# Kernel optimization log

Measured on AMD Instinct MI355X. Metric: run time of the kernel, lower is better.

Reference implementation:

```python
import jax, jax.numpy as jnp
import numpy as np
from jax import lax

B, T = 64, 2048
ENC, DEC, ATT = 512, 1024, 128
NFILT, KSIZE = 32, 31
PAD = KSIZE // 2


def setup_inputs() -> dict:
    key = jax.random.key(0)
    ks = jax.random.split(key, 9)
    query = jax.random.normal(ks[0], (B, 1, DEC), dtype=jnp.float32)
    keys = jax.random.normal(ks[1], (B, T, ENC), dtype=jnp.float32)
    prev_weights = jax.random.uniform(ks[2], (B, T), dtype=jnp.float32)
    mask = jax.random.randint(ks[3], (B, T), 0, 2, dtype=jnp.int32)
    # params stored as [in, out] (transpose of torch Linear weight); same math
    W1 = jax.random.normal(ks[4], (ENC, ATT), dtype=jnp.float32) * (ENC ** -0.5)
    W2 = jax.random.normal(ks[5], (DEC, ATT), dtype=jnp.float32) * (DEC ** -0.5)
    V = jax.random.normal(ks[6], (ATT,), dtype=jnp.float32) * (ATT ** -0.5)
    conv_w = jax.random.normal(ks[7], (NFILT, 1, KSIZE), dtype=jnp.float32) * (KSIZE ** -0.5)
    loc_dense = jax.random.normal(ks[8], (NFILT, ATT), dtype=jnp.float32) * (NFILT ** -0.5)
    return {"query": query, "keys": keys, "prev_weights": prev_weights, "mask": mask,
            "W1": W1, "W2": W2, "V": V, "conv_w": conv_w, "loc_dense": loc_dense}


def reference(query, keys, prev_weights, mask, W1, W2, V, conv_w, loc_dense):
    proj_key = jnp.einsum('bte,ea->bta', keys, W1)          # [B,T,A]
    proj_query = jnp.einsum('bqd,da->bqa', query, W2)       # [B,1,A]
    # location conv: input [B,1,T], kernel [F,1,K], 'same' padding -> [B,F,T]
    loc_feat = lax.conv_general_dilated(prev_weights[:, None, :], conv_w,
                                        window_strides=(1,), padding=[(PAD, PAD)],
                                        dimension_numbers=('NCH', 'OIH', 'NCH'))
    proj_loc = jnp.einsum('bft,fa->bta', loc_feat, loc_dense)  # [B,T,A]
    scores = jnp.einsum('bta,a->bt', jnp.tanh(proj_key + proj_query + proj_loc), V)
    scores = jnp.where(mask == 0, -1e9, scores)
    weights = jax.nn.softmax(scores, axis=-1)                # [B,T]
    context = jnp.einsum('bt,bte->be', weights, keys)[:, None, :]  # [B,1,ENC]
    return context, weights
```

## Files before the change

### kernel.cpp

```cpp
#include <hip/hip_runtime.h>

typedef __attribute__((ext_vector_type(4))) float f32x4;
typedef __attribute__((ext_vector_type(8))) short bf16x8;

#define T_LEN 2048
#define ENC   512
#define DEC   1024
#define ATT   128
#define NB    64
#define BM    128
#define BK    32
#define NXB   (T_LEN / BM)
#define NSTEP 17

typedef unsigned int u32;
typedef __attribute__((address_space(1))) const u32 gu32;
typedef __attribute__((address_space(3))) u32 lu32;

__device__ __forceinline__ void async_copy16(const float* g, float* l) {
  __builtin_amdgcn_global_load_lds((gu32*)g, (lu32*)l, 16, 0, 0);
}

__device__ __forceinline__ unsigned short f2bf_rne(float x) {
  unsigned int u = __builtin_bit_cast(unsigned int, x);
  u += 0x7fff + ((u >> 16) & 1);
  return (unsigned short)(u >> 16);
}
__device__ __forceinline__ short f2bf_fast(float x) {
  unsigned int u = __builtin_bit_cast(unsigned int, x);
  return (short)((u + 0x8000u) >> 16);
}

__device__ __forceinline__ float fast_tanh(float x) {
  float e = __expf(2.f * x);
  return 1.f - 2.f / (e + 1.f);
}

__global__ __launch_bounds__(128) void prep(
    const float* __restrict__ query, const float* __restrict__ W2,
    const float* __restrict__ W1, const float* __restrict__ convw,
    const float* __restrict__ ldense,
    float* __restrict__ pq, unsigned short* __restrict__ Bl) {
  int bidx = blockIdx.x;
  if (bidx < NB) {
    int a = threadIdx.x;
    float acc = 0.f;
    for (int d = 0; d < DEC; ++d) acc += query[bidx * DEC + d] * W2[d * ATT + a];
    pq[bidx * ATT + a] = acc;
  } else {
    int a = bidx - NB;
    for (int k = threadIdx.x; k < NSTEP * BK; k += 128) {
      float v = 0.f;
      if (k < 512) {
        v = W1[k * ATT + a];
      } else if (k < 543) {
        int kc = k - 512;
        #pragma unroll
        for (int f = 0; f < 32; ++f) v += convw[f * 31 + kc] * ldense[f * ATT + a];
      }
      int kt = k >> 5, kk = k & 31;
      Bl[(kt * 128 + a) * BK + kk] = f2bf_rne(v);
    }
  }
}

__global__ __launch_bounds__(256, 4) void lsa_main(
    const float* __restrict__ keys, const float* __restrict__ prev,
    const int* __restrict__ mask, const unsigned short* __restrict__ Bl,
    const float* __restrict__ pq, const float* __restrict__ Vv,
    float* __restrict__ wout, float* __restrict__ dpart, float* __restrict__ cpart) {
  __shared__ float Abf[2][BM * BK];
  __shared__ float s_red[2][BM];
  __shared__ float e_vals[BM];

  const int tid = threadIdx.x;
  const int b = blockIdx.y;
  const int trow0 = blockIdx.x * BM;
  const int bid = b * NXB + blockIdx.x;

  const int lane = tid & 63;
  const int w = tid >> 6;
  const int wr = w >> 1, wc = w & 1;
  const int rsel = lane & 15, grp = lane >> 4;

  const int lr = lane >> 3, cp = lane & 7;
  const int gr = w * 32 + lr;
  const int gc = cp ^ lr;
  const float* gA = keys + ((size_t)b * T_LEN + trow0 + gr) * ENC + gc * 4;

  const unsigned short* gB = Bl + (size_t)(wc * 64 + rsel) * BK + grp * 8;

  const int rx = rsel & 7;
  const int ca0 = (2 * grp) ^ rx, ca1 = (2 * grp + 1) ^ rx;
  const int arow_base = (wr * 64 + rsel) * BK;

  f32x4 acc[4][4];
  #pragma unroll
  for (int m = 0; m < 4; ++m)
    #pragma unroll
    for (int n = 0; n < 4; ++n) acc[m][n] = (f32x4)0.f;

  #pragma unroll
  for (int i = 0; i < 4; ++i)
    async_copy16(gA + (size_t)i * 8 * ENC, &Abf[0][(w * 4 + i) * 256]);
  __syncthreads();

  for (int t = 0; t < 16; ++t) {
    if (t < 15) {
      const float* gt = gA + (t + 1) * BK;
      float* dst = &Abf[(t + 1) & 1][0];
      #pragma unroll
      for (int i = 0; i < 4; ++i)
        async_copy16(gt + (size_t)i * 8 * ENC, &dst[(w * 4 + i) * 256]);
    } else {
      const int r = tid >> 1, kh = tid & 1;
      const int rx2 = r & 7;
      float* dst = &Abf[0][r * BK];
      #pragma unroll
      for (int jc = 0; jc < 4; ++jc) {
        int c = kh * 4 + jc;
        f32x4 v;
        #pragma unroll
        for (int q = 0; q < 4; ++q) {
          int kk = c * 4 + q;
          int pos = trow0 + r + kk - 15;
          v[q] = (kk < 31 && pos >= 0 && pos < T_LEN) ? prev[b * T_LEN + pos] : 0.f;
        }
        *reinterpret_cast<f32x4*>(&dst[(c ^ rx2) * 4]) = v;
      }
    }
    bf16x8 bfr[4];
    {
      const unsigned short* gBt = gB + (size_t)t * (128 * BK);
      #pragma unroll
      for (int n = 0; n < 4; ++n)
        bfr[n] = *reinterpret_cast<const bf16x8*>(gBt + n * 16 * BK);
    }
    {
      const float* Ab = &Abf[t & 1][0];
      #pragma unroll
      for (int m = 0; m < 4; ++m) {
        f32x4 x0 = *reinterpret_cast<const f32x4*>(&Ab[arow_base + m * 16 * BK + ca0 * 4]);
        f32x4 x1 = *reinterpret_cast<const f32x4*>(&Ab[arow_base + m * 16 * BK + ca1 * 4]);
        bf16x8 af;
        #pragma unroll
        for (int j = 0; j < 4; ++j) { af[j] = f2bf_fast(x0[j]); af[4 + j] = f2bf_fast(x1[j]); }
        #pragma unroll
        for (int n = 0; n < 4; ++n)
          acc[m][n] = __builtin_amdgcn_mfma_f32_16x16x32_bf16(af, bfr[n], acc[m][n], 0, 0, 0);
      }
    }
    __syncthreads();
  }
  {
    bf16x8 bfr[4];
    const unsigned short* gBt = gB + (size_t)16 * (128 * BK);
    #pragma unroll
    for (int n = 0; n < 4; ++n)
      bfr[n] = *reinterpret_cast<const bf16x8*>(gBt + n * 16 * BK);
    const float* Ab = &Abf[0][0];
    #pragma unroll
    for (int m = 0; m < 4; ++m) {
      f32x4 x0 = *reinterpret_cast<const f32x4*>(&Ab[arow_base + m * 16 * BK + ca0 * 4]);
      f32x4 x1 = *reinterpret_cast<const f32x4*>(&Ab[arow_base + m * 16 * BK + ca1 * 4]);
      bf16x8 af;
      #pragma unroll
      for (int j = 0; j < 4; ++j) { af[j] = f2bf_fast(x0[j]); af[4 + j] = f2bf_fast(x1[j]); }
      #pragma unroll
      for (int n = 0; n < 4; ++n)
        acc[m][n] = __builtin_amdgcn_mfma_f32_16x16x32_bf16(af, bfr[n], acc[m][n], 0, 0, 0);
    }
  }

  float psum[4][4];
  #pragma unroll
  for (int m = 0; m < 4; ++m)
    #pragma unroll
    for (int i = 0; i < 4; ++i) psum[m][i] = 0.f;
  #pragma unroll
  for (int n = 0; n < 4; ++n) {
    int c = wc * 64 + n * 16 + rsel;
    float pqv = pq[b * ATT + c];
    float vv = Vv[c];
    #pragma unroll
    for (int m = 0; m < 4; ++m)
      #pragma unroll
      for (int i = 0; i < 4; ++i)
        psum[m][i] += vv * fast_tanh(acc[m][n][i] + pqv);
  }
  #pragma unroll
  for (int m = 0; m < 4; ++m)
    #pragma unroll
    for (int i = 0; i < 4; ++i) {
      float v = psum[m][i];
      v += __shfl_xor(v, 1, 64);
      v += __shfl_xor(v, 2, 64);
      v += __shfl_xor(v, 4, 64);
      v += __shfl_xor(v, 8, 64);
      psum[m][i] = v;
    }
  if (rsel == 0) {
    #pragma unroll
    for (int m = 0; m < 4; ++m)
      #pragma unroll
      for (int i = 0; i < 4; ++i)
        s_red[wc][wr * 64 + m * 16 + grp * 4 + i] = psum[m][i];
  }
  __syncthreads();

  if (tid < BM) {
    int trow = trow0 + tid;
    float s = s_red[0][tid] + s_red[1][tid];
    float e = (mask[b * T_LEN + trow] == 0) ? 0.f : __expf(s);
    wout[b * T_LEN + trow] = e;
    e_vals[tid] = e;
  }
  __syncthreads();

  if (tid < 64) {
    float v = e_vals[tid] + e_vals[tid + 64];
    #pragma unroll
    for (int off = 32; off; off >>= 1) v += __shfl_xor(v, off, 64);
    if (tid == 0) dpart[bid] = v;
  }

  float c0 = 0.f, c1 = 0.f;
  const float* krow = keys + ((size_t)b * T_LEN + trow0) * ENC;
  #pragma unroll 4
  for (int r = 0; r < BM; ++r) {
    float e = e_vals[r];
    if (e != 0.f) {
      c0 += e * krow[(size_t)r * ENC + tid];
      c1 += e * krow[(size_t)r * ENC + tid + 256];
    }
  }
  cpart[(size_t)bid * ENC + tid] = c0;
  cpart[(size_t)bid * ENC + tid + 256] = c1;
}

__global__ __launch_bounds__(256) void lsa_finalize(
    const float* __restrict__ dpart, const float* __restrict__ cpart,
    float* __restrict__ out) {
  int b = blockIdx.x, tid = threadIdx.x;
  float d = 0.f;
  #pragma unroll
  for (int i = 0; i < NXB; ++i) d += dpart[b * NXB + i];
  float inv = 1.f / d;
  for (int e = tid; e < ENC; e += 256) {
    float c = 0.f;
    #pragma unroll
    for (int i = 0; i < NXB; ++i) c += cpart[((size_t)(b * NXB + i)) * ENC + e];
    out[b * ENC + e] = c * inv;
  }
  float* wrow = out + NB * ENC + (size_t)b * T_LEN;
  for (int t = tid; t < T_LEN; t += 256) wrow[t] *= inv;
}

extern "C" void kernel_launch(void* const* d_in, const int* in_sizes, int n_in,
                              void* d_out, int out_size, void* d_ws, size_t ws_size,
                              hipStream_t stream) {
  const float* query  = (const float*)d_in[0];
  const float* keys   = (const float*)d_in[1];
  const float* prev   = (const float*)d_in[2];
  const int*   mask   = (const int*)d_in[3];
  const float* W1     = (const float*)d_in[4];
  const float* W2     = (const float*)d_in[5];
  const float* V      = (const float*)d_in[6];
  const float* convw  = (const float*)d_in[7];
  const float* ldense = (const float*)d_in[8];
  float* out = (float*)d_out;

  char* ws = (char*)d_ws;
  unsigned short* Bl = (unsigned short*)ws;
  float* pq    = (float*)(ws + 139264);
  float* dpart = (float*)(ws + 139264 + 32768);
  float* cpart = (float*)(ws + 139264 + 32768 + 4096);

  prep<<<dim3(192), dim3(128), 0, stream>>>(query, W2, W1, convw, ldense, pq, Bl);
  dim3 grid(NXB, NB);
  lsa_main<<<grid, dim3(256), 0, stream>>>(keys, prev, mask, Bl, pq, V,
                                           out + NB * ENC, dpart, cpart);
  lsa_finalize<<<dim3(NB), dim3(256), 0, stream>>>(dpart, cpart, out);
}
```

Measured before the change: 135.5 us.

## Unroll GEMM K-loop by two with register-prefetched B fragments; vectorize context accumulation

The main K loop is unrolled by two with ping-pong register buffers for the B fragments, so the next step's B loads are issued before the current MFMA block runs. The context pass now loads two adjacent floats per thread with a vector load and drops the branch that skipped masked rows. The query projection in prep is split across four accumulators to shorten its dependency chain. The changes trade extra registers and code size for better latency hiding, and the context pass now also reads keys for masked rows.

Measured after the change: 134.9 us. Within noise of the previous version (-0.4%).

```diff
diff --git a/kernel.cpp b/kernel.cpp
--- a/kernel.cpp
+++ b/kernel.cpp
@@ -1,6 +1,7 @@
 #include <hip/hip_runtime.h>
 
 typedef __attribute__((ext_vector_type(4))) float f32x4;
+typedef __attribute__((ext_vector_type(2))) float f32x2;
 typedef __attribute__((ext_vector_type(8))) short bf16x8;
 
 #define T_LEN 2048
@@ -11,7 +12,6 @@
 #define BM    128
 #define BK    32
 #define NXB   (T_LEN / BM)
-#define NSTEP 17
 
 typedef unsigned int u32;
 typedef __attribute__((address_space(1))) const u32 gu32;
@@ -44,12 +44,18 @@
   int bidx = blockIdx.x;
   if (bidx < NB) {
     int a = threadIdx.x;
-    float acc = 0.f;
-    for (int d = 0; d < DEC; ++d) acc += query[bidx * DEC + d] * W2[d * ATT + a];
-    pq[bidx * ATT + a] = acc;
+    const float* q = query + bidx * DEC;
+    float a0 = 0.f, a1 = 0.f, a2 = 0.f, a3 = 0.f;
+    for (int d = 0; d < DEC; d += 4) {
+      a0 += q[d]     * W2[(d)     * ATT + a];
+      a1 += q[d + 1] * W2[(d + 1) * ATT + a];
+      a2 += q[d + 2] * W2[(d + 2) * ATT + a];
+      a3 += q[d + 3] * W2[(d + 3) * ATT + a];
+    }
+    pq[bidx * ATT + a] = (a0 + a1) + (a2 + a3);
   } else {
     int a = bidx - NB;
-    for (int k = threadIdx.x; k < NSTEP * BK; k += 128) {
+    for (int k = threadIdx.x; k < 17 * BK; k += 128) {
       float v = 0.f;
       if (k < 512) {
         v = W1[k * ATT + a];
@@ -100,77 +106,68 @@
     #pragma unroll
     for (int n = 0; n < 4; ++n) acc[m][n] = (f32x4)0.f;
 
-  #pragma unroll
-  for (int i = 0; i < 4; ++i)
-    async_copy16(gA + (size_t)i * 8 * ENC, &Abf[0][(w * 4 + i) * 256]);
+#define STAGE(t_, buf_) do { \
+    const float* gt_ = gA + (t_) * BK; \
+    float* dst_ = &Abf[buf_][0]; \
+    _Pragma("unroll") \
+    for (int i_ = 0; i_ < 4; ++i_) \
+      async_copy16(gt_ + (size_t)i_ * 8 * ENC, &dst_[(w * 4 + i_) * 256]); } while (0)
+
+#define STAGE_CONV() do { \
+    const int r_ = tid >> 1, kh_ = tid & 1; \
+    const int rx2_ = r_ & 7; \
+    float* dst_ = &Abf[0][r_ * BK]; \
+    _Pragma("unroll") \
+    for (int jc_ = 0; jc_ < 4; ++jc_) { \
+      int c_ = kh_ * 4 + jc_; \
+      f32x4 v_; \
+      _Pragma("unroll") \
+      for (int q_ = 0; q_ < 4; ++q_) { \
+        int kk_ = c_ * 4 + q_; \
+        int pos_ = trow0 + r_ + kk_ - 15; \
+        v_[q_] = (kk_ < 31 && pos_ >= 0 && pos_ < T_LEN) ? prev[b * T_LEN + pos_] : 0.f; \
+      } \
+      *reinterpret_cast<f32x4*>(&dst_[(c_ ^ rx2_) * 4]) = v_; \
+    } } while (0)
+
+#define LOADB(dst_, t_) do { \
+    const unsigned short* gBt_ = gB + (size_t)(t_) * (128 * BK); \
+    dst_[0] = *reinterpret_cast<const bf16x8*>(gBt_); \
+    dst_[1] = *reinterpret_cast<const bf16x8*>(gBt_ + 16 * BK); \
+    dst_[2] = *reinterpret_cast<const bf16x8*>(gBt_ + 32 * BK); \
+    dst_[3] = *reinterpret_cast<const bf16x8*>(gBt_ + 48 * BK); } while (0)
+
+#define COMPUTE(buf_, br_) do { \
+    const float* Ab_ = &Abf[buf_][0]; \
+    _Pragma("unroll") \
+    for (int m_ = 0; m_ < 4; ++m_) { \
+      f32x4 x0_ = *reinterpret_cast<const f32x4*>(&Ab_[arow_base + m_ * 16 * BK + ca0 * 4]); \
+      f32x4 x1_ = *reinterpret_cast<const f32x4*>(&Ab_[arow_base + m_ * 16 * BK + ca1 * 4]); \
+      bf16x8 af_; \
+      _Pragma("unroll") \
+      for (int j_ = 0; j_ < 4; ++j_) { af_[j_] = f2bf_fast(x0_[j_]); af_[4 + j_] = f2bf_fast(x1_[j_]); } \
+      _Pragma("unroll") \
+      for (int n_ = 0; n_ < 4; ++n_) \
+        acc[m_][n_] = __builtin_amdgcn_mfma_f32_16x16x32_bf16(af_, br_[n_], acc[m_][n_], 0, 0, 0); \
+    } } while (0)
+
+  bf16x8 bA[4], bB[4];
+  STAGE(0, 0);
+  LOADB(bA, 0);
   __syncthreads();
 
-  for (int t = 0; t < 16; ++t) {
-    if (t < 15) {
-      const float* gt = gA + (t + 1) * BK;
-      float* dst = &Abf[(t + 1) & 1][0];
-      #pragma unroll
-      for (int i = 0; i < 4; ++i)
-        async_copy16(gt + (size_t)i * 8 * ENC, &dst[(w * 4 + i) * 256]);
-    } else {
-      const int r = tid >> 1, kh = tid & 1;
-      const int rx2 = r & 7;
-      float* dst = &Abf[0][r * BK];
-      #pragma unroll
-      for (int jc = 0; jc < 4; ++jc) {
-        int c = kh * 4 + jc;
-        f32x4 v;
-        #pragma unroll
-        for (int q = 0; q < 4; ++q) {
-          int kk = c * 4 + q;
-          int pos = trow0 + r + kk - 15;
-          v[q] = (kk < 31 && pos >= 0 && pos < T_LEN) ? prev[b * T_LEN + pos] : 0.f;
-        }
-        *reinterpret_cast<f32x4*>(&dst[(c ^ rx2) * 4]) = v;
-      }
-    }
-    bf16x8 bfr[4];
-    {
-      const unsigned short* gBt = gB + (size_t)t * (128 * BK);
-      #pragma unroll
-      for (int n = 0; n < 4; ++n)
-        bfr[n] = *reinterpret_cast<const bf16x8*>(gBt + n * 16 * BK);
-    }
-    {
-      const float* Ab = &Abf[t & 1][0];
-      #pragma unroll
-      for (int m = 0; m < 4; ++m) {
-        f32x4 x0 = *reinterpret_cast<const f32x4*>(&Ab[arow_base + m * 16 * BK + ca0 * 4]);
-        f32x4 x1 = *reinterpret_cast<const f32x4*>(&Ab[arow_base + m * 16 * BK + ca1 * 4]);
-        bf16x8 af;
-        #pragma unroll
-        for (int j = 0; j < 4; ++j) { af[j] = f2bf_fast(x0[j]); af[4 + j] = f2bf_fast(x1[j]); }
-        #pragma unroll
-        for (int n = 0; n < 4; ++n)
-          acc[m][n] = __builtin_amdgcn_mfma_f32_16x16x32_bf16(af, bfr[n], acc[m][n], 0, 0, 0);
-      }
-    }
+  #pragma unroll
+  for (int tt = 0; tt < 16; tt += 2) {
+    LOADB(bB, tt + 1);
+    STAGE(tt + 1, 1);
+    COMPUTE(0, bA);
     __syncthreads();
-  }
-  {
-    bf16x8 bfr[4];
-    const unsigned short* gBt = gB + (size_t)16 * (128 * BK);
-    #pragma unroll
-    for (int n = 0; n < 4; ++n)
-      bfr[n] = *reinterpret_cast<const bf16x8*>(gBt + n * 16 * BK);
-    const float* Ab = &Abf[0][0];
-    #pragma unroll
-    for (int m = 0; m < 4; ++m) {
-      f32x4 x0 = *reinterpret_cast<const f32x4*>(&Ab[arow_base + m * 16 * BK + ca0 * 4]);
-      f32x4 x1 = *reinterpret_cast<const f32x4*>(&Ab[arow_base + m * 16 * BK + ca1 * 4]);
-      bf16x8 af;
-      #pragma unroll
-      for (int j = 0; j < 4; ++j) { af[j] = f2bf_fast(x0[j]); af[4 + j] = f2bf_fast(x1[j]); }
-      #pragma unroll
-      for (int n = 0; n < 4; ++n)
-        acc[m][n] = __builtin_amdgcn_mfma_f32_16x16x32_bf16(af, bfr[n], acc[m][n], 0, 0, 0);
-    }
-  }
+    LOADB(bA, tt + 2);
+    if (tt < 14) STAGE(tt + 2, 0); else STAGE_CONV();
+    COMPUTE(1, bB);
+    __syncthreads();
+  }
+  COMPUTE(0, bA);
 
   float psum[4][4];
   #pragma unroll
@@ -224,18 +221,18 @@
     if (tid == 0) dpart[bid] = v;
   }
 
-  float c0 = 0.f, c1 = 0.f;
-  const float* krow = keys + ((size_t)b * T_LEN + trow0) * ENC;
-  #pragma unroll 4
-  for (int r = 0; r < BM; ++r) {
-    float e = e_vals[r];
-    if (e != 0.f) {
-      c0 += e * krow[(size_t)r * ENC + tid];
-      c1 += e * krow[(size_t)r * ENC + tid + 256];
-    }
-  }
-  cpart[(size_t)bid * ENC + tid] = c0;
-  cpart[(size_t)bid * ENC + tid + 256] = c1;
+  {
+    const float* kcol = keys + ((size_t)b * T_LEN + trow0) * ENC + 2 * tid;
+    f32x2 cacc; cacc.x = 0.f; cacc.y = 0.f;
+    #pragma unroll 8
+    for (int r = 0; r < BM; ++r) {
+      float e = e_vals[r];
+      f32x2 kv = *reinterpret_cast<const f32x2*>(kcol + (size_t)r * ENC);
+      cacc.x += e * kv.x;
+      cacc.y += e * kv.y;
+    }
+    *reinterpret_cast<f32x2*>(cpart + (size_t)bid * ENC + 2 * tid) = cacc;
+  }
 }
 
 __global__ __launch_bounds__(256) void lsa_finalize(
```
